# Optimization experiments

Hardware: AMD Instinct MI355X
Metric: run time of the kernel (lower is better)

The kernel has to match this reference:

```python
import jax, jax.numpy as jnp
import numpy as np

MASK_PENALTY = 1000.0
K = 1  # default k in bds_loss


def setup_inputs() -> dict:
    key = jax.random.key(0)
    k1, k2, k3, k4, k5, k6 = jax.random.split(key, 6)
    bt, nv, nf, H, W, S = 4, 20000, 40000, 256, 256, 2048
    verts = jax.random.normal(k1, (bt, nv, 3), dtype=jnp.float32)
    bds_xyz = jax.random.normal(k2, (bt, S, 3), dtype=jnp.float32)
    bds_mask = (jax.random.uniform(k3, (bt, S, 1)) < 0.7).astype(jnp.float32)
    bds = jnp.concatenate([bds_xyz, bds_mask], axis=-1)  # [bt,S,4]
    faces = jax.random.randint(k4, (bt, nf, 3), 0, nv, dtype=jnp.int64)
    p2f = jax.random.randint(k5, (bt, H, W, 1), 0, bt * nf, dtype=jnp.int64)
    bg = jax.random.uniform(k6, (bt, H, W, 1)) < 0.3
    pix_to_face = jnp.where(bg, jnp.int64(-1), p2f)
    return {"verts": verts, "bds": bds, "faces": faces,
            "pix_to_face": pix_to_face, "n_samples": S}


def _bds_loss(verts, bds, faces, pix_to_face, n_samples, k=K):
    bt, nv, _ = verts.shape
    # subsample boundary points (order-invariant -> identity indexing)
    bds_v = bds[:, :n_samples, :-1]   # [bt,S,3]
    bds_m = bds[:, :n_samples, -1]    # [bt,S]

    # ---- visibility mask from rasterized face indices ----
    fi = pix_to_face[..., 0].reshape(-1)                       # [bt*H*W]
    offs = jnp.arange(bt, dtype=faces.dtype)[:, None, None] * nv
    faces_packed = (faces + offs).reshape(-1, 3)               # [bt*nf,3]
    valid = fi >= 0
    fi_safe = jnp.where(valid, fi, 0)
    sel = faces_packed[fi_safe]                                # [bt*HW,3]
    vals = jnp.broadcast_to(valid[:, None], sel.shape).astype(verts.dtype)
    visible = jnp.zeros(bt * nv, dtype=verts.dtype).at[sel.reshape(-1)].max(vals.reshape(-1))
    visible = visible.reshape(bt, nv)                          # [bt,nv], 0/1

    # ---- squared pairwise distances: cdist(bds_v, verts)**2 ----
    d2 = (jnp.sum(bds_v * bds_v, -1)[:, :, None]
          + jnp.sum(verts * verts, -1)[:, None, :]
          - 2.0 * jnp.einsum('bsd,bvd->bsv', bds_v, verts))   # [bt,S,nv]

    dist = (1.0 - visible[:, None, :]) * MASK_PENALTY + visible[:, None, :] * d2
    min_dists = -jax.lax.top_k(-dist, k)[0]                    # [bt,S,k] smallest-k

    loss = (min_dists * bds_m[:, :, None]).mean(-1).sum(-1)    # [bt]
    return loss.mean()


def reference(verts, bds, faces, pix_to_face, n_samples):
    return _bds_loss(verts, bds, faces, pix_to_face, n_samples)
```

## Files before the change

### kernel.cpp

```cpp
#include <hip/hip_runtime.h>

#define BT   4
#define NV   20000
#define NF   40000
#define SMP  2048
#define NPIX (BT * 256 * 256)
#define NVG  (BT * NV)
#define NCH  64
#define CHUNK ((NV + NCH - 1) / NCH)
#define P    8

__device__ __forceinline__ unsigned int enc_f32(float f) {
    unsigned int u = __float_as_uint(f);
    return (u & 0x80000000u) ? ~u : (u | 0x80000000u);
}
__device__ __forceinline__ float dec_f32(unsigned int k) {
    unsigned int u = (k & 0x80000000u) ? (k & 0x7FFFFFFFu) : ~k;
    return __uint_as_float(u);
}

__global__ void init_k(unsigned int* __restrict__ minKeys,
                       int* __restrict__ flags,
                       float* __restrict__ visible) {
    int i = blockIdx.x * blockDim.x + threadIdx.x;
    if (i < BT * SMP) minKeys[i] = 0xFFFFFFFFu;
    if (i < BT)       flags[i]   = 0;
    if (i < NVG)      visible[i] = 0.0f;
}

__global__ void vis_k(const int* __restrict__ p2f,
                      const int* __restrict__ faces,
                      float* __restrict__ visible) {
    int p = blockIdx.x * blockDim.x + threadIdx.x;
    if (p >= NPIX) return;
    int fi = p2f[p];
    if (fi < 0) return;
    int b    = fi / NF;
    int base = fi * 3;
    int off  = b * NV;
    visible[faces[base + 0] + off] = 1.0f;
    visible[faces[base + 1] + off] = 1.0f;
    visible[faces[base + 2] + off] = 1.0f;
}

__global__ void pack_k(const float* __restrict__ verts,
                       const float* __restrict__ visible,
                       float4* __restrict__ packed,
                       int* __restrict__ flags) {
    int i = blockIdx.x * blockDim.x + threadIdx.x;
    if (i >= NVG) return;
    float x = verts[3 * i + 0];
    float y = verts[3 * i + 1];
    float z = verts[3 * i + 2];
    float w;
    if (visible[i] > 0.0f) {
        w = x * x + y * y + z * z;
    } else {
        w = 1e30f;
        flags[i / NV] = 1;
    }
    packed[i] = make_float4(-2.0f * x, -2.0f * y, -2.0f * z, w);
}

__global__ __launch_bounds__(256) void
main_k(const float4* __restrict__ bds,
       const float4* __restrict__ packed,
       unsigned int* __restrict__ minKeys) {
    __shared__ float4 sh[256];
    const int b  = blockIdx.z;
    const int v0 = blockIdx.x * CHUNK;
    const int v1 = min(v0 + CHUNK, NV);

    float px[P], py[P], pz[P], mn[P];
    #pragma unroll
    for (int u = 0; u < P; ++u) {
        float4 p = bds[b * SMP + u * 256 + threadIdx.x];
        px[u] = p.x; py[u] = p.y; pz[u] = p.z;
        mn[u] = 3.0e38f;
    }

    const float4* vp = packed + b * NV;
    for (int t = v0; t < v1; t += 256) {
        int idx = t + threadIdx.x;
        if (idx < v1) sh[threadIdx.x] = vp[idx];
        __syncthreads();
        int cnt = min(256, v1 - t);
        #pragma unroll 2
        for (int j = 0; j < cnt; ++j) {
            float4 v = sh[j];
            #pragma unroll
            for (int u = 0; u < P; ++u) {
                float q = fmaf(px[u], v.x,
                          fmaf(py[u], v.y,
                          fmaf(pz[u], v.z, v.w)));
                mn[u] = fminf(mn[u], q);
            }
        }
        __syncthreads();
    }
    #pragma unroll
    for (int u = 0; u < P; ++u)
        atomicMin(&minKeys[b * SMP + u * 256 + threadIdx.x], enc_f32(mn[u]));
}

__global__ void red_k(const unsigned int* __restrict__ minKeys,
                      const float4* __restrict__ bds,
                      const int* __restrict__ flags,
                      float* __restrict__ out) {
    const int tid = threadIdx.x;
    float sum = 0.0f;
    for (int i = tid; i < BT * SMP; i += 1024) {
        int b = i >> 11;
        float4 p = bds[i];
        float bs = p.x * p.x + p.y * p.y + p.z * p.z;
        float mn = dec_f32(minKeys[i]) + bs;
        if (flags[b]) mn = fminf(mn, 1000.0f);
        sum = fmaf(mn, p.w, sum);
    }
    #pragma unroll
    for (int o = 32; o > 0; o >>= 1) sum += __shfl_down(sum, o, 64);
    __shared__ float part[16];
    if ((tid & 63) == 0) part[tid >> 6] = sum;
    __syncthreads();
    if (tid == 0) {
        float t = 0.0f;
        #pragma unroll
        for (int i = 0; i < 16; ++i) t += part[i];
        out[0] = t / (float)BT;
    }
}

extern "C" void kernel_launch(void* const* d_in, const int* in_sizes, int n_in,
                              void* d_out, int out_size, void* d_ws, size_t ws_size,
                              hipStream_t stream) {
    const float* verts = (const float*)d_in[0];
    const float* bds   = (const float*)d_in[1];
    const int*   faces = (const int*)d_in[2];
    const int*   p2f   = (const int*)d_in[3];
    float*       out   = (float*)d_out;

    char* ws = (char*)d_ws;
    unsigned int* minKeys = (unsigned int*)ws;
    int*    flags   = (int*)(ws + 32768);
    float4* packed  = (float4*)(ws + 32800);
    float*  visible = (float*)(ws + 32800 + 1280000);

    init_k<<<(NVG + 255) / 256, 256, 0, stream>>>(minKeys, flags, visible);
    vis_k<<<(NPIX + 255) / 256, 256, 0, stream>>>(p2f, faces, visible);
    pack_k<<<(NVG + 255) / 256, 256, 0, stream>>>(verts, visible, packed, flags);
    main_k<<<dim3(NCH, 1, BT), 256, 0, stream>>>(
        (const float4*)bds, packed, minKeys);
    red_k<<<1, 1024, 0, stream>>>(minKeys, (const float4*)bds, flags, out);
}
```

Baseline: 103.0 us.

## Double vertex chunks, replace atomicMin with per-chunk partials and multi-block reduction

Doubles the number of vertex chunks so the main distance kernel launches twice as many blocks. Each block now writes its per-sample minima to a dedicated slice instead of doing encoded atomicMin. A 32-block reduction kernel mins across chunks and combines the sums with an atomic-add/counter finish. The visibility kernel reads four pixels per thread via int4, and the inner loop unroll rises to 4. This removes the minKey init and atomics at the cost of a 4 MB partial buffer and a longer reduction pass.

Result: slower. 112.2 us (+9.0%).

```diff
diff --git a/kernel.cpp b/kernel.cpp
--- a/kernel.cpp
+++ b/kernel.cpp
@@ -6,41 +6,39 @@
 #define SMP  2048
 #define NPIX (BT * 256 * 256)
 #define NVG  (BT * NV)
-#define NCH  64
+#define NCH  128
 #define CHUNK ((NV + NCH - 1) / NCH)
 #define P    8
+#define RED_BLOCKS 32
 
-__device__ __forceinline__ unsigned int enc_f32(float f) {
-    unsigned int u = __float_as_uint(f);
-    return (u & 0x80000000u) ? ~u : (u | 0x80000000u);
-}
-__device__ __forceinline__ float dec_f32(unsigned int k) {
-    unsigned int u = (k & 0x80000000u) ? (k & 0x7FFFFFFFu) : ~k;
-    return __uint_as_float(u);
+__global__ void init_k(float* __restrict__ visible,
+                       int* __restrict__ flags,
+                       float* __restrict__ acc,
+                       unsigned int* __restrict__ cnt) {
+    int i = blockIdx.x * blockDim.x + threadIdx.x;
+    if (i < NVG) visible[i] = 0.0f;
+    if (i < BT)  flags[i]   = 0;
+    if (i == 0) { acc[0] = 0.0f; cnt[0] = 0u; }
 }
 
-__global__ void init_k(unsigned int* __restrict__ minKeys,
-                       int* __restrict__ flags,
-                       float* __restrict__ visible) {
-    int i = blockIdx.x * blockDim.x + threadIdx.x;
-    if (i < BT * SMP) minKeys[i] = 0xFFFFFFFFu;
-    if (i < BT)       flags[i]   = 0;
-    if (i < NVG)      visible[i] = 0.0f;
-}
-
-__global__ void vis_k(const int* __restrict__ p2f,
+__global__ void vis_k(const int4* __restrict__ p2f,
                       const int* __restrict__ faces,
                       float* __restrict__ visible) {
     int p = blockIdx.x * blockDim.x + threadIdx.x;
-    if (p >= NPIX) return;
-    int fi = p2f[p];
-    if (fi < 0) return;
-    int b    = fi / NF;
-    int base = fi * 3;
-    int off  = b * NV;
-    visible[faces[base + 0] + off] = 1.0f;
-    visible[faces[base + 1] + off] = 1.0f;
-    visible[faces[base + 2] + off] = 1.0f;
+    int4 f4 = p2f[p];
+    int fs[4] = {f4.x, f4.y, f4.z, f4.w};
+    #pragma unroll
+    for (int k = 0; k < 4; ++k) {
+        int fi = fs[k];
+        if (fi >= 0) {
+            int b    = fi / NF;
+            int base = fi * 3;
+            int off  = b * NV;
+            visible[faces[base + 0] + off] = 1.0f;
+            visible[faces[base + 1] + off] = 1.0f;
+            visible[faces[base + 2] + off] = 1.0f;
+        }
+    }
 }
 
 __global__ void pack_k(const float* __restrict__ verts,
@@ -65,10 +63,11 @@
 __global__ __launch_bounds__(256) void
 main_k(const float4* __restrict__ bds,
        const float4* __restrict__ packed,
-       unsigned int* __restrict__ minKeys) {
+       float* __restrict__ mnOut) {
     __shared__ float4 sh[256];
     const int b  = blockIdx.z;
-    const int v0 = blockIdx.x * CHUNK;
+    const int c  = blockIdx.x;
+    const int v0 = c * CHUNK;
     const int v1 = min(v0 + CHUNK, NV);
 
     float px[P], py[P], pz[P], mn[P];
@@ -85,7 +84,7 @@
         if (idx < v1) sh[threadIdx.x] = vp[idx];
         __syncthreads();
         int cnt = min(256, v1 - t);
-        #pragma unroll 2
+        #pragma unroll 4
         for (int j = 0; j < cnt; ++j) {
             float4 v = sh[j];
             #pragma unroll
@@ -98,35 +97,45 @@
         }
         __syncthreads();
     }
+    float* dst = mnOut + c * (BT * SMP) + b * SMP;
     #pragma unroll
     for (int u = 0; u < P; ++u)
-        atomicMin(&minKeys[b * SMP + u * 256 + threadIdx.x], enc_f32(mn[u]));
+        dst[u * 256 + threadIdx.x] = mn[u];
 }
 
-__global__ void red_k(const unsigned int* __restrict__ minKeys,
-                      const float4* __restrict__ bds,
-                      const int* __restrict__ flags,
-                      float* __restrict__ out) {
-    const int tid = threadIdx.x;
-    float sum = 0.0f;
-    for (int i = tid; i < BT * SMP; i += 1024) {
-        int b = i >> 11;
-        float4 p = bds[i];
-        float bs = p.x * p.x + p.y * p.y + p.z * p.z;
-        float mn = dec_f32(minKeys[i]) + bs;
-        if (flags[b]) mn = fminf(mn, 1000.0f);
-        sum = fmaf(mn, p.w, sum);
-    }
+__global__ __launch_bounds__(256) void
+red_k(const float* __restrict__ mnOut,
+      const float4* __restrict__ bds,
+      const int* __restrict__ flags,
+      float* __restrict__ acc,
+      unsigned int* __restrict__ cnt,
+      float* __restrict__ out) {
+    const int i = blockIdx.x * 256 + threadIdx.x;
+    const int b = i >> 11;
+    float4 p = bds[i];
+    float v = mnOut[i];
+    #pragma unroll 8
+    for (int c = 1; c < NCH; ++c)
+        v = fminf(v, mnOut[c * (BT * SMP) + i]);
+    float bs = fmaf(p.x, p.x, fmaf(p.y, p.y, p.z * p.z));
+    float mn = v + bs;
+    if (flags[b]) mn = fminf(mn, 1000.0f);
+    float contrib = mn * p.w;
+
     #pragma unroll
-    for (int o = 32; o > 0; o >>= 1) sum += __shfl_down(sum, o, 64);
-    __shared__ float part[16];
-    if ((tid & 63) == 0) part[tid >> 6] = sum;
+    for (int o = 32; o > 0; o >>= 1) contrib += __shfl_down(contrib, o, 64);
+    __shared__ float part[4];
+    if ((threadIdx.x & 63) == 0) part[threadIdx.x >> 6] = contrib;
     __syncthreads();
-    if (tid == 0) {
-        float t = 0.0f;
-        #pragma unroll
-        for (int i = 0; i < 16; ++i) t += part[i];
-        out[0] = t / (float)BT;
+    if (threadIdx.x == 0) {
+        float t = part[0] + part[1] + part[2] + part[3];
+        atomicAdd(acc, t);
+        __threadfence();
+        unsigned int n = atomicAdd(cnt, 1u);
+        if (n == RED_BLOCKS - 1) {
+            __threadfence();
+            out[0] = *((volatile float*)acc) / (float)BT;
+        }
     }
 }
 
@@ -140,15 +149,19 @@
     float*       out   = (float*)d_out;
 
     char* ws = (char*)d_ws;
-    unsigned int* minKeys = (unsigned int*)ws;
-    int*    flags   = (int*)(ws + 32768);
-    float4* packed  = (float4*)(ws + 32800);
-    float*  visible = (float*)(ws + 32800 + 1280000);
+    float*  mnOut   = (float*)ws;
+    float4* packed  = (float4*)(ws + 4194304);
+    float*  visible = (float*)(ws + 4194304 + 1280000);
+    int*    flags   = (int*)(ws + 4194304 + 1280000 + 320000);
+    float*  acc     = (float*)(ws + 4194304 + 1280000 + 320016);
+    unsigned int* cnt = (unsigned int*)(ws + 4194304 + 1280000 + 320020);
 
-    init_k<<<(NVG + 255) / 256, 256, 0, stream>>>(minKeys, flags, visible);
-    vis_k<<<(NPIX + 255) / 256, 256, 0, stream>>>(p2f, faces, visible);
+    init_k<<<(NVG + 255) / 256, 256, 0, stream>>>(visible, flags, acc, cnt);
+    vis_k<<<(NPIX / 4 + 255) / 256, 256, 0, stream>>>(
+        (const int4*)p2f, faces, visible);
     pack_k<<<(NVG + 255) / 256, 256, 0, stream>>>(verts, visible, packed, flags);
     main_k<<<dim3(NCH, 1, BT), 256, 0, stream>>>(
-        (const float4*)bds, packed, minKeys);
-    red_k<<<1, 1024, 0, stream>>>(minKeys, (const float4*)bds, flags, out);
+        (const float4*)bds, packed, mnOut);
+    red_k<<<RED_BLOCKS, 256, 0, stream>>>(
+        mnOut, (const float4*)bds, flags, acc, cnt, out);
 }
```
